# Optimization experiments

Hardware: AMD Instinct MI355X
Metric: run time of the kernel (lower is better)

The kernel has to match this reference:

```python
import jax, jax.numpy as jnp
import numpy as np

N = 10000
E = 640000
F = 128      # in_dim
H = 4        # heads
Dh = 32      # head_dim = ceil(128/4)
INNER = H * Dh   # 128 == out_dim -> W_out is Identity
OUT = 128
SCALE = 1.0 / np.sqrt(float(Dh))
LN_EPS = 1e-5


def setup_inputs() -> dict:
    key = jax.random.key(0)
    ks = jax.random.split(key, 8)
    s = 1.0 / np.sqrt(F)
    nodes = jax.random.normal(ks[0], (N, F), dtype=jnp.float32)
    edge_index = jax.random.randint(ks[1], (2, E), 0, N, dtype=jnp.int32)
    W_Q = jax.random.uniform(ks[2], (F, INNER), jnp.float32, -s, s)
    W_K = jax.random.uniform(ks[3], (F, INNER), jnp.float32, -s, s)
    W_V = jax.random.uniform(ks[4], (F, INNER), jnp.float32, -s, s)
    W_res = jax.random.uniform(ks[5], (F, OUT), jnp.float32, -s, s)
    b_res = jax.random.uniform(ks[6], (OUT,), jnp.float32, -s, s)
    gamma = jnp.ones((OUT,), jnp.float32)
    beta = jnp.zeros((OUT,), jnp.float32)
    return {"nodes": nodes, "W_Q": W_Q, "W_K": W_K, "W_V": W_V,
            "W_res": W_res, "b_res": b_res, "gamma": gamma, "beta": beta,
            "edge_index": edge_index}


def reference(nodes, W_Q, W_K, W_V, W_res, b_res, gamma, beta, edge_index):
    n = nodes.shape[0]
    src = edge_index[0]
    dst = edge_index[1]
    # node-level projections, split into heads: [N, H, Dh]
    Q = (nodes @ W_Q).reshape(n, H, Dh)
    K = (nodes @ W_K).reshape(n, H, Dh)
    V = (nodes @ W_V).reshape(n, H, Dh)
    # per-edge gathers: q from dst, k/v from src
    q = Q[dst]          # [E, H, Dh]
    k = K[src]
    v = V[src]
    score = jnp.sum(q * k, axis=-1) * SCALE      # [E, H]
    # segment softmax over dst
    mx = jax.ops.segment_max(score, dst, num_segments=n)   # [N, H]
    mx = jnp.where(jnp.isfinite(mx), mx, 0.0)               # guard empty segments
    ex = jnp.exp(score - mx[dst])                           # [E, H]
    sm = jax.ops.segment_sum(ex, dst, num_segments=n)       # [N, H]
    alpha = ex / (sm[dst] + 1e-12)                          # [E, H]
    # scatter-aggregate weighted values
    agg = jax.ops.segment_sum(alpha[:, :, None] * v, dst, num_segments=n)  # [N, H, Dh]
    H_cat = agg.reshape(n, INNER)                # W_out is Identity (inner == out)
    H_out = H_cat + nodes @ W_res + b_res        # residual projection
    # LayerNorm(out_dim)
    mu = jnp.mean(H_out, axis=-1, keepdims=True)
    var = jnp.mean(jnp.square(H_out - mu), axis=-1, keepdims=True)
    x_hat = (H_out - mu) * jax.lax.rsqrt(var + LN_EPS)
    return gamma * x_hat + beta
```

## Files before the change

### kernel.cpp

```cpp
#include <hip/hip_runtime.h>
#include <math.h>

#define FDIM 128
#define NP 64
#define NMAX 10240
static constexpr float SC2 = 0.17677669529663687f * 1.4426950408889634f;
static constexpr float LN_EPS = 1e-5f;

typedef __attribute__((ext_vector_type(8))) short bf16x8;
typedef __attribute__((ext_vector_type(4))) float f32x4;

__device__ __forceinline__ unsigned short f2bf(float f) {
    unsigned u = __float_as_uint(f);
    unsigned r = u + 0x7FFFu + ((u >> 16) & 1u);
    return (unsigned short)(r >> 16);
}

__global__ __launch_bounds__(256) void prep_kernel(
    const float* __restrict__ Wq, const float* __restrict__ Wk,
    const float* __restrict__ Wv, const float* __restrict__ Wr,
    unsigned short* __restrict__ Wt)
{
    const int tid = threadIdx.x;
    const int t = blockIdx.x;
    const int wiW = t >> 2, q = t & 3;
    const float* __restrict__ W = (wiW == 0) ? Wq : (wiW == 1) ? Wk : (wiW == 2) ? Wv : Wr;
    const int c = q * 32 + (tid >> 3);
    const int k0 = (tid & 7) * 16;
    unsigned short* dp = &Wt[(size_t)wiW * 16384 + c * 128 + k0];
    #pragma unroll
    for (int kk = 0; kk < 16; ++kk)
        dp[kk] = f2bf(W[(k0 + kk) * FDIM + c]);
}

__global__ __launch_bounds__(256) void gemm_hist_kernel(
    const float* __restrict__ nodes,
    const unsigned short* __restrict__ Wt,
    const float* __restrict__ br,
    unsigned short* __restrict__ Qu, unsigned short* __restrict__ KVu,
    float* __restrict__ Rb, int N,
    const int* __restrict__ dst, int* __restrict__ bh,
    int* __restrict__ rank, int E, int C)
{
    __shared__ __align__(16) char smem[52224];
    const int tid = threadIdx.x;
    const int wi = blockIdx.y;

    if (wi == 0) {
        const int p = blockIdx.x;
        if (p >= NP) return;
        int* h = (int*)smem;
        for (int i = tid; i < N; i += 256) h[i] = 0;
        __syncthreads();
        const int lo = p * C;
        const int hi = min(lo + C, E);
        const int n = hi - lo;
        if (n > 0) {
            if (((lo | E) & 3) == 0) {
                const int4* d4 = (const int4*)(dst + lo);
                int4* r4p = (int4*)(rank + lo);
                const int n4 = n >> 2;
                for (int i = tid; i < n4; i += 256) {
                    int4 d = d4[i];
                    int4 r;
                    r.x = atomicAdd(&h[d.x], 1);
                    r.y = atomicAdd(&h[d.y], 1);
                    r.z = atomicAdd(&h[d.z], 1);
                    r.w = atomicAdd(&h[d.w], 1);
                    r4p[i] = r;
                }
                for (int i = lo + (n4 << 2) + tid; i < hi; i += 256)
                    rank[i] = atomicAdd(&h[dst[i]], 1);
            } else {
                for (int i = lo + tid; i < hi; i += 256)
                    rank[i] = atomicAdd(&h[dst[i]], 1);
            }
        }
        __syncthreads();
        for (int i = tid; i < N; i += 256) bh[p * N + i] = h[i];
        return;
    }

    const int gw = wi - 1;
    const int row0 = blockIdx.x * 64;
    unsigned short (*As)[136] = (unsigned short(*)[136])smem;
    unsigned short (*Ws)[136] = (unsigned short(*)[136])(smem + 64 * 272);

    #pragma unroll
    for (int i = 0; i < 8; ++i) {
        const int idx = tid + i * 256;
        const int r = idx >> 5, c4 = idx & 31;
        const int gr = row0 + r;
        float4 v = make_float4(0.f, 0.f, 0.f, 0.f);
        if (gr < N) v = *reinterpret_cast<const float4*>(&nodes[(size_t)gr * FDIM + c4 * 4]);
        ushort4 o;
        o.x = f2bf(v.x); o.y = f2bf(v.y); o.z = f2bf(v.z); o.w = f2bf(v.w);
        *reinterpret_cast<ushort4*>(&As[r][c4 * 4]) = o;
    }
    const unsigned short* Wg = &Wt[(size_t)gw * 16384];
    #pragma unroll
    for (int i = 0; i < 8; ++i) {
        const int idx = tid + i * 256;
        const int r = idx >> 4, ch = idx & 15;
        const uint4 v = *reinterpret_cast<const uint4*>(&Wg[r * 128 + ch * 8]);
        *reinterpret_cast<uint4*>(&Ws[r][ch * 8]) = v;
    }
    __syncthreads();

    const int w = tid >> 6;
    const int l = tid & 63;
    const int lr = l & 15;
    const int lh = l >> 4;

    f32x4 acc[8];
    #pragma unroll
    for (int ct = 0; ct < 8; ++ct) acc[ct] = (f32x4){0.f, 0.f, 0.f, 0.f};

    #pragma unroll
    for (int kc = 0; kc < 4; ++kc) {
        const bf16x8 a = *reinterpret_cast<const bf16x8*>(&As[w * 16 + lr][kc * 32 + lh * 8]);
        #pragma unroll
        for (int ct = 0; ct < 8; ++ct) {
            const bf16x8 bb = *reinterpret_cast<const bf16x8*>(&Ws[ct * 16 + lr][kc * 32 + lh * 8]);
            acc[ct] = __builtin_amdgcn_mfma_f32_16x16x32_bf16(a, bb, acc[ct], 0, 0, 0);
        }
    }

    const int rbase = row0 + w * 16 + lh * 4;
    #pragma unroll
    for (int ct = 0; ct < 8; ++ct) {
        const int col = ct * 16 + lr;
        float bc = 0.f;
        if (gw == 3) bc = br[col];
        #pragma unroll
        for (int r = 0; r < 4; ++r) {
            const int row = rbase + r;
            if (row >= N) continue;
            const float val = acc[ct][r];
            if (gw == 0)      Qu[(size_t)row * 128 + col] = f2bf(val);
            else if (gw == 1) KVu[(size_t)row * 256 + col] = f2bf(val);
            else if (gw == 2) KVu[(size_t)row * 256 + 128 + col] = f2bf(val);
            else              Rb[(size_t)row * 128 + col] = val + bc;
        }
    }
}

__global__ __launch_bounds__(256) void degrel_kernel(
    int* __restrict__ bh, int* __restrict__ deg, int N)
{
    const int d = blockIdx.x * 256 + threadIdx.x;
    if (d < N) {
        int c = 0;
        #pragma unroll
        for (int p = 0; p < NP; ++p) {
            const int cnt = bh[p * N + d];
            bh[p * N + d] = c;
            c += cnt;
        }
        deg[d] = c;
    }
}

__global__ __launch_bounds__(1024) void scan_kernel(
    const int* __restrict__ deg, int* __restrict__ rowptr, int N)
{
    __shared__ int tot[NMAX];
    __shared__ int wsum[16];
    const int tid = threadIdx.x;
    const int lane = tid & 63;
    const int wid = tid >> 6;

    for (int d = tid; d < N; d += 1024) tot[d] = deg[d];
    __syncthreads();

    const int CH = (N + 1023) / 1024;
    const int b = tid * CH;
    const int e = min(b + CH, N);
    int s = 0;
    for (int i = b; i < e; ++i) s += tot[i];

    int incl = s;
    #pragma unroll
    for (int off = 1; off < 64; off <<= 1) {
        int t = __shfl_up(incl, off);
        if (lane >= off) incl += t;
    }
    if (lane == 63) wsum[wid] = incl;
    __syncthreads();
    if (wid == 0) {
        int v = (lane < 16) ? wsum[lane] : 0;
        #pragma unroll
        for (int off = 1; off < 16; off <<= 1) {
            int t = __shfl_up(v, off);
            if (lane >= off) v += t;
        }
        if (lane < 16) wsum[lane] = v;
    }
    __syncthreads();
    const int wbase = (wid > 0) ? wsum[wid - 1] : 0;
    int run = wbase + incl - s;
    for (int i = b; i < e; ++i) {
        const int t = tot[i];
        rowptr[i] = run;
        run += t;
    }
    if (tid == 1023) rowptr[N] = wsum[15];
}

__global__ __launch_bounds__(256) void scatter_kernel(
    const int* __restrict__ src, const int* __restrict__ dst,
    const int* __restrict__ rank, const int* __restrict__ rel,
    const int* __restrict__ rowptr, int* __restrict__ ssrc,
    int N, int E, int C)
{
    const int p = blockIdx.x >> 3;
    const int sub = blockIdx.x & 7;
    const int CS = C >> 3;
    const int lo = p * C + sub * CS;
    const int hi = min(lo + CS, E);
    const int n = hi - lo;
    if (n <= 0) return;
    const int* rp = &rel[p * N];

    if (((lo | E) & 3) == 0) {
        const int4* s4 = (const int4*)(src + lo);
        const int4* d4 = (const int4*)(dst + lo);
        const int4* r4 = (const int4*)(rank + lo);
        const int n4 = n >> 2;
        for (int i = threadIdx.x; i < n4; i += 256) {
            const int4 s = s4[i];
            const int4 d = d4[i];
            const int4 r = r4[i];
            ssrc[rowptr[d.x] + rp[d.x] + r.x] = s.x;
            ssrc[rowptr[d.y] + rp[d.y] + r.y] = s.y;
            ssrc[rowptr[d.z] + rp[d.z] + r.z] = s.z;
            ssrc[rowptr[d.w] + rp[d.w] + r.w] = s.w;
        }
        for (int i = lo + (n4 << 2) + threadIdx.x; i < hi; i += 256)
            ssrc[rowptr[dst[i]] + rp[dst[i]] + rank[i]] = src[i];
    } else {
        for (int i = lo + threadIdx.x; i < hi; i += 256)
            ssrc[rowptr[dst[i]] + rp[dst[i]] + rank[i]] = src[i];
    }
}

__global__ __launch_bounds__(256) void agg_kernel(
    const unsigned short* __restrict__ Qu, const unsigned short* __restrict__ KVu,
    const float* __restrict__ Rb,
    const int* __restrict__ rowptr, const int* __restrict__ ssrc,
    const float* __restrict__ gamma, const float* __restrict__ beta,
    float* __restrict__ out, int N)
{
    const int wave = threadIdx.x >> 6;
    const int lane = threadIdx.x & 63;
    const int qtr = lane >> 4;
    const int lq = lane & 15;
    const int n = blockIdx.x * 16 + wave * 4 + qtr;
    if (n >= N) return;
    const int d0 = lq * 8;

    const uint4 qu = *reinterpret_cast<const uint4*>(&Qu[(size_t)n * 128 + d0]);
    const float qf0 = __uint_as_float(qu.x << 16), qf1 = __uint_as_float(qu.x & 0xFFFF0000u);
    const float qf2 = __uint_as_float(qu.y << 16), qf3 = __uint_as_float(qu.y & 0xFFFF0000u);
    const float qf4 = __uint_as_float(qu.z << 16), qf5 = __uint_as_float(qu.z & 0xFFFF0000u);
    const float qf6 = __uint_as_float(qu.w << 16), qf7 = __uint_as_float(qu.w & 0xFFFF0000u);

    const int beg = rowptr[n];
    const int end = rowptr[n + 1];

    float4 A0a = make_float4(0.f, 0.f, 0.f, 0.f), A0b = A0a;
    float4 A1a = A0a, A1b = A0a, A2a = A0a, A2b = A0a, A3a = A0a, A3b = A0a;
    float L0 = 0.f, L1 = 0.f, L2 = 0.f, L3 = 0.f;

#define GATHER(S, NK, NV)                                                     \
    {                                                                         \
        const unsigned short* bp = &KVu[(size_t)(S) * 256 + d0];              \
        NK = *reinterpret_cast<const uint4*>(bp);                             \
        NV = *reinterpret_cast<const uint4*>(bp + 128);                       \
    }
#define STEP(KU, VU, Aa, Ab, L)                                               \
    {                                                                         \
        const float k0 = __uint_as_float((KU).x << 16), k1 = __uint_as_float((KU).x & 0xFFFF0000u); \
        const float k2 = __uint_as_float((KU).y << 16), k3 = __uint_as_float((KU).y & 0xFFFF0000u); \
        const float k4 = __uint_as_float((KU).z << 16), k5 = __uint_as_float((KU).z & 0xFFFF0000u); \
        const float k6 = __uint_as_float((KU).w << 16), k7 = __uint_as_float((KU).w & 0xFFFF0000u); \
        float p = qf0 * k0 + qf1 * k1 + qf2 * k2 + qf3 * k3                   \
                + qf4 * k4 + qf5 * k5 + qf6 * k6 + qf7 * k7;                  \
        p += __shfl_xor(p, 1);                                                \
        p += __shfl_xor(p, 2);                                                \
        const float e1 = exp2f(p * SC2);                                      \
        const float v0 = __uint_as_float((VU).x << 16), v1 = __uint_as_float((VU).x & 0xFFFF0000u); \
        const float v2 = __uint_as_float((VU).y << 16), v3 = __uint_as_float((VU).y & 0xFFFF0000u); \
        const float v4 = __uint_as_float((VU).z << 16), v5 = __uint_as_float((VU).z & 0xFFFF0000u); \
        const float v6 = __uint_as_float((VU).w << 16), v7 = __uint_as_float((VU).w & 0xFFFF0000u); \
        Aa.x += e1 * v0; Aa.y += e1 * v1; Aa.z += e1 * v2; Aa.w += e1 * v3;   \
        Ab.x += e1 * v4; Ab.y += e1 * v5; Ab.z += e1 * v6; Ab.w += e1 * v7;   \
        L += e1;                                                              \
    }

    uint4 nk0, nv0, nk1, nv1, nk2, nv2, nk3, nv3;
    int j = beg;
    const int nb = (end - beg) >> 2;
    if (nb > 0) {
        int c0i = ssrc[j], c1i = ssrc[j + 1], c2i = ssrc[j + 2], c3i = ssrc[j + 3];
        GATHER(c0i, nk0, nv0); GATHER(c1i, nk1, nv1);
        GATHER(c2i, nk2, nv2); GATHER(c3i, nk3, nv3);
        int x0 = ssrc[j + 4], x1 = ssrc[j + 5], x2 = ssrc[j + 6], x3 = ssrc[j + 7];
        for (int bi = 1; bi < nb; ++bi) {
            const uint4 ck0 = nk0, cv0 = nv0, ck1 = nk1, cv1 = nv1;
            const uint4 ck2 = nk2, cv2 = nv2, ck3 = nk3, cv3 = nv3;
            c0i = x0; c1i = x1; c2i = x2; c3i = x3;
            const int nbase = j + (bi + 1) * 4;
            x0 = ssrc[nbase]; x1 = ssrc[nbase + 1];
            x2 = ssrc[nbase + 2]; x3 = ssrc[nbase + 3];
            GATHER(c0i, nk0, nv0); GATHER(c1i, nk1, nv1);
            GATHER(c2i, nk2, nv2); GATHER(c3i, nk3, nv3);
            STEP(ck0, cv0, A0a, A0b, L0);
            STEP(ck1, cv1, A1a, A1b, L1);
            STEP(ck2, cv2, A2a, A2b, L2);
            STEP(ck3, cv3, A3a, A3b, L3);
        }
        STEP(nk0, nv0, A0a, A0b, L0);
        STEP(nk1, nv1, A1a, A1b, L1);
        STEP(nk2, nv2, A2a, A2b, L2);
        STEP(nk3, nv3, A3a, A3b, L3);
        j = beg + nb * 4;
    }
    for (; j < end; ++j) {
        const int s0 = ssrc[j];
        uint4 k0u, v0u;
        GATHER(s0, k0u, v0u);
        STEP(k0u, v0u, A0a, A0b, L0);
    }
#undef GATHER
#undef STEP

    const float L = (L0 + L1) + (L2 + L3);
    const float inv = 1.f / (L + 1e-12f);
    const float4 ra = *reinterpret_cast<const float4*>(&Rb[(size_t)n * 128 + d0]);
    const float4 rb = *reinterpret_cast<const float4*>(&Rb[(size_t)n * 128 + d0 + 4]);
    float xa0 = ((A0a.x + A1a.x) + (A2a.x + A3a.x)) * inv + ra.x;
    float xa1 = ((A0a.y + A1a.y) + (A2a.y + A3a.y)) * inv + ra.y;
    float xa2 = ((A0a.z + A1a.z) + (A2a.z + A3a.z)) * inv + ra.z;
    float xa3 = ((A0a.w + A1a.w) + (A2a.w + A3a.w)) * inv + ra.w;
    float xb0 = ((A0b.x + A1b.x) + (A2b.x + A3b.x)) * inv + rb.x;
    float xb1 = ((A0b.y + A1b.y) + (A2b.y + A3b.y)) * inv + rb.y;
    float xb2 = ((A0b.z + A1b.z) + (A2b.z + A3b.z)) * inv + rb.z;
    float xb3 = ((A0b.w + A1b.w) + (A2b.w + A3b.w)) * inv + rb.w;

    float s1v = (xa0 + xa1 + xa2 + xa3) + (xb0 + xb1 + xb2 + xb3);
    float s2v = xa0 * xa0 + xa1 * xa1 + xa2 * xa2 + xa3 * xa3
              + xb0 * xb0 + xb1 * xb1 + xb2 * xb2 + xb3 * xb3;
    #pragma unroll
    for (int off = 8; off; off >>= 1) {
        s1v += __shfl_xor(s1v, off);
        s2v += __shfl_xor(s2v, off);
    }
    const float mu = s1v * (1.f / 128.f);
    float var = s2v * (1.f / 128.f) - mu * mu;
    var = fmaxf(var, 0.f);
    const float rs = rsqrtf(var + LN_EPS);

    const float4 ga = *reinterpret_cast<const float4*>(&gamma[d0]);
    const float4 gb = *reinterpret_cast<const float4*>(&gamma[d0 + 4]);
    const float4 ba = *reinterpret_cast<const float4*>(&beta[d0]);
    const float4 bb = *reinterpret_cast<const float4*>(&beta[d0 + 4]);
    float4 oa, ob;
    oa.x = ga.x * (xa0 - mu) * rs + ba.x;
    oa.y = ga.y * (xa1 - mu) * rs + ba.y;
    oa.z = ga.z * (xa2 - mu) * rs + ba.z;
    oa.w = ga.w * (xa3 - mu) * rs + ba.w;
    ob.x = gb.x * (xb0 - mu) * rs + bb.x;
    ob.y = gb.y * (xb1 - mu) * rs + bb.y;
    ob.z = gb.z * (xb2 - mu) * rs + bb.z;
    ob.w = gb.w * (xb3 - mu) * rs + bb.w;
    *reinterpret_cast<float4*>(&out[(size_t)n * 128 + d0]) = oa;
    *reinterpret_cast<float4*>(&out[(size_t)n * 128 + d0 + 4]) = ob;
}

extern "C" void kernel_launch(void* const* d_in, const int* in_sizes, int n_in,
                              void* d_out, int out_size, void* d_ws, size_t ws_size,
                              hipStream_t stream)
{
    const float* nodes = (const float*)d_in[0];
    const float* W_Q   = (const float*)d_in[1];
    const float* W_K   = (const float*)d_in[2];
    const float* W_V   = (const float*)d_in[3];
    const float* W_res = (const float*)d_in[4];
    const float* b_res = (const float*)d_in[5];
    const float* gamma = (const float*)d_in[6];
    const float* beta  = (const float*)d_in[7];
    const int*   eidx  = (const int*)d_in[8];

    const int N = in_sizes[0] / FDIM;
    const int E = in_sizes[8] / 2;
    const int* src = eidx;
    const int* dst = eidx + E;

    float* out = (float*)d_out;

    unsigned short* KVu = (unsigned short*)d_ws;
    unsigned short* Qu  = KVu + (size_t)N * 256;
    unsigned short* Wt  = Qu + (size_t)N * 128;
    float* Rb   = (float*)(Wt + 4 * 16384);
    int* bh     = (int*)(Rb + (size_t)N * 128);
    int* rowptr = bh + (size_t)NP * N;
    int* deg    = rowptr + (N + 1);
    int* rank   = deg + N;
    int* ssrc   = rank + E;

    const int C = (((E + NP - 1) / NP) + 31) & ~31;
    const int nG = (N + 63) / 64;
    const int nB = (N + 255) / 256;

    prep_kernel<<<16, 256, 0, stream>>>(W_Q, W_K, W_V, W_res, Wt);

    dim3 ggrid(nG, 5);
    gemm_hist_kernel<<<ggrid, 256, 0, stream>>>(nodes, Wt, b_res,
                                                Qu, KVu, Rb, N, dst, bh, rank, E, C);
    degrel_kernel<<<nB, 256, 0, stream>>>(bh, deg, N);
    scan_kernel<<<1, 1024, 0, stream>>>(deg, rowptr, N);
    scatter_kernel<<<NP * 8, 256, 0, stream>>>(src, dst, rank, bh, rowptr, ssrc, N, E, C);
    agg_kernel<<<(N + 15) / 16, 256, 0, stream>>>(Qu, KVu, Rb, rowptr, ssrc,
                                                  gamma, beta, out, N);
}
```

Before: 91.68 us.

## Split each node's edge list across two quarter-waves and combine via shared memory

The aggregation kernel now assigns two 16-lane groups to each destination node. Each group processes half of the 4-edge blocks, and the odd group handles the remainder edges. Partial softmax numerators and denominators are combined through LDS after a block barrier, and the launch grid doubles to 8 nodes per block. This raises memory-level parallelism and shortens per-node serial gather chains (about 64 edges per node). The cost is an extra __syncthreads, shared-memory traffic, and a second pipeline prologue and epilogue per node.

```diff
diff --git a/kernel.cpp b/kernel.cpp
--- a/kernel.cpp
+++ b/kernel.cpp
@@ -251,22 +251,37 @@
     const float* __restrict__ gamma, const float* __restrict__ beta,
     float* __restrict__ out, int N)
 {
+    __shared__ float sA[8][16][8];
+    __shared__ float sL[8][16];
+
     const int wave = threadIdx.x >> 6;
     const int lane = threadIdx.x & 63;
     const int qtr = lane >> 4;
     const int lq = lane & 15;
-    const int n = blockIdx.x * 16 + wave * 4 + qtr;
-    if (n >= N) return;
+    const int slot = wave * 2 + (qtr >> 1);
+    const int s = qtr & 1;
+    const int n = blockIdx.x * 8 + slot;
+    const bool active = (n < N);
     const int d0 = lq * 8;
 
-    const uint4 qu = *reinterpret_cast<const uint4*>(&Qu[(size_t)n * 128 + d0]);
+    uint4 qu = make_uint4(0u, 0u, 0u, 0u);
+    int beg = 0, end = 0;
+    if (active) {
+        qu = *reinterpret_cast<const uint4*>(&Qu[(size_t)n * 128 + d0]);
+        beg = rowptr[n];
+        end = rowptr[n + 1];
+    }
     const float qf0 = __uint_as_float(qu.x << 16), qf1 = __uint_as_float(qu.x & 0xFFFF0000u);
     const float qf2 = __uint_as_float(qu.y << 16), qf3 = __uint_as_float(qu.y & 0xFFFF0000u);
     const float qf4 = __uint_as_float(qu.z << 16), qf5 = __uint_as_float(qu.z & 0xFFFF0000u);
     const float qf6 = __uint_as_float(qu.w << 16), qf7 = __uint_as_float(qu.w & 0xFFFF0000u);
 
-    const int beg = rowptr[n];
-    const int end = rowptr[n + 1];
+    const int nbAll = (end - beg) >> 2;
+    const int nbh = (nbAll + 1) >> 1;
+    const int b0 = (s == 0) ? 0 : nbh;
+    const int b1 = (s == 0) ? nbh : nbAll;
+    const int j0 = beg + b0 * 4;
+    const int m = b1 - b0;
 
     float4 A0a = make_float4(0.f, 0.f, 0.f, 0.f), A0b = A0a;
     float4 A1a = A0a, A1b = A0a, A2a = A0a, A2b = A0a, A3a = A0a, A3b = A0a;
@@ -299,18 +314,16 @@
     }
 
     uint4 nk0, nv0, nk1, nv1, nk2, nv2, nk3, nv3;
-    int j = beg;
-    const int nb = (end - beg) >> 2;
-    if (nb > 0) {
-        int c0i = ssrc[j], c1i = ssrc[j + 1], c2i = ssrc[j + 2], c3i = ssrc[j + 3];
+    if (m > 0) {
+        int c0i = ssrc[j0], c1i = ssrc[j0 + 1], c2i = ssrc[j0 + 2], c3i = ssrc[j0 + 3];
         GATHER(c0i, nk0, nv0); GATHER(c1i, nk1, nv1);
         GATHER(c2i, nk2, nv2); GATHER(c3i, nk3, nv3);
-        int x0 = ssrc[j + 4], x1 = ssrc[j + 5], x2 = ssrc[j + 6], x3 = ssrc[j + 7];
-        for (int bi = 1; bi < nb; ++bi) {
+        int x0 = ssrc[j0 + 4], x1 = ssrc[j0 + 5], x2 = ssrc[j0 + 6], x3 = ssrc[j0 + 7];
+        for (int bi = 1; bi < m; ++bi) {
             const uint4 ck0 = nk0, cv0 = nv0, ck1 = nk1, cv1 = nv1;
             const uint4 ck2 = nk2, cv2 = nv2, ck3 = nk3, cv3 = nv3;
             c0i = x0; c1i = x1; c2i = x2; c3i = x3;
-            const int nbase = j + (bi + 1) * 4;
+            const int nbase = j0 + (bi + 1) * 4;
             x0 = ssrc[nbase]; x1 = ssrc[nbase + 1];
             x2 = ssrc[nbase + 2]; x3 = ssrc[nbase + 3];
             GATHER(c0i, nk0, nv0); GATHER(c1i, nk1, nv1);
@@ -324,29 +337,55 @@
         STEP(nk1, nv1, A1a, A1b, L1);
         STEP(nk2, nv2, A2a, A2b, L2);
         STEP(nk3, nv3, A3a, A3b, L3);
-        j = beg + nb * 4;
-    }
-    for (; j < end; ++j) {
-        const int s0 = ssrc[j];
-        uint4 k0u, v0u;
-        GATHER(s0, k0u, v0u);
-        STEP(k0u, v0u, A0a, A0b, L0);
+    }
+    if (s == 1) {
+        for (int j = beg + nbAll * 4; j < end; ++j) {
+            const int s0 = ssrc[j];
+            uint4 k0u, v0u;
+            GATHER(s0, k0u, v0u);
+            STEP(k0u, v0u, A0a, A0b, L0);
+        }
     }
 #undef GATHER
 #undef STEP
 
-    const float L = (L0 + L1) + (L2 + L3);
+    float a0 = (A0a.x + A1a.x) + (A2a.x + A3a.x);
+    float a1 = (A0a.y + A1a.y) + (A2a.y + A3a.y);
+    float a2 = (A0a.z + A1a.z) + (A2a.z + A3a.z);
+    float a3 = (A0a.w + A1a.w) + (A2a.w + A3a.w);
+    float a4 = (A0b.x + A1b.x) + (A2b.x + A3b.x);
+    float a5 = (A0b.y + A1b.y) + (A2b.y + A3b.y);
+    float a6 = (A0b.z + A1b.z) + (A2b.z + A3b.z);
+    float a7 = (A0b.w + A1b.w) + (A2b.w + A3b.w);
+    float L = (L0 + L1) + (L2 + L3);
+
+    if (s == 1) {
+        float* dp = &sA[slot][lq][0];
+        dp[0] = a0; dp[1] = a1; dp[2] = a2; dp[3] = a3;
+        dp[4] = a4; dp[5] = a5; dp[6] = a6; dp[7] = a7;
+        sL[slot][lq] = L;
+    }
+    __syncthreads();
+    if (s == 1 || !active) return;
+
+    {
+        const float* dp = &sA[slot][lq][0];
+        a0 += dp[0]; a1 += dp[1]; a2 += dp[2]; a3 += dp[3];
+        a4 += dp[4]; a5 += dp[5]; a6 += dp[6]; a7 += dp[7];
+        L += sL[slot][lq];
+    }
+
     const float inv = 1.f / (L + 1e-12f);
     const float4 ra = *reinterpret_cast<const float4*>(&Rb[(size_t)n * 128 + d0]);
     const float4 rb = *reinterpret_cast<const float4*>(&Rb[(size_t)n * 128 + d0 + 4]);
-    float xa0 = ((A0a.x + A1a.x) + (A2a.x + A3a.x)) * inv + ra.x;
-    float xa1 = ((A0a.y + A1a.y) + (A2a.y + A3a.y)) * inv + ra.y;
-    float xa2 = ((A0a.z + A1a.z) + (A2a.z + A3a.z)) * inv + ra.z;
-    float xa3 = ((A0a.w + A1a.w) + (A2a.w + A3a.w)) * inv + ra.w;
-    float xb0 = ((A0b.x + A1b.x) + (A2b.x + A3b.x)) * inv + rb.x;
-    float xb1 = ((A0b.y + A1b.y) + (A2b.y + A3b.y)) * inv + rb.y;
-    float xb2 = ((A0b.z + A1b.z) + (A2b.z + A3b.z)) * inv + rb.z;
-    float xb3 = ((A0b.w + A1b.w) + (A2b.w + A3b.w)) * inv + rb.w;
+    float xa0 = a0 * inv + ra.x;
+    float xa1 = a1 * inv + ra.y;
+    float xa2 = a2 * inv + ra.z;
+    float xa3 = a3 * inv + ra.w;
+    float xb0 = a4 * inv + rb.x;
+    float xb1 = a5 * inv + rb.y;
+    float xb2 = a6 * inv + rb.z;
+    float xb3 = a7 * inv + rb.w;
 
     float s1v = (xa0 + xa1 + xa2 + xa3) + (xb0 + xb1 + xb2 + xb3);
     float s2v = xa0 * xa0 + xa1 * xa1 + xa2 * xa2 + xa3 * xa3
@@ -421,6 +460,6 @@
     degrel_kernel<<<nB, 256, 0, stream>>>(bh, deg, N);
     scan_kernel<<<1, 1024, 0, stream>>>(deg, rowptr, N);
     scatter_kernel<<<NP * 8, 256, 0, stream>>>(src, dst, rank, bh, rowptr, ssrc, N, E, C);
-    agg_kernel<<<(N + 15) / 16, 256, 0, stream>>>(Qu, KVu, Rb, rowptr, ssrc,
-                                                  gamma, beta, out, N);
-}
+    agg_kernel<<<(N + 7) / 8, 256, 0, stream>>>(Qu, KVu, Rb, rowptr, ssrc,
+                                                gamma, beta, out, N);
+}
```

Result: faster. 89.34 us (-2.6%).
